# Kernel optimization log

Measured on AMD Instinct MI355X. Metric: run time of the kernel, lower is better.

Reference implementation:

```python
import jax, jax.numpy as jnp
import numpy as np

NUM_NODES = 1_000_000
MEM_DIM = 100
TIME_DIM = 100
MSG_DIM = 4
OUT_CH = 2
BATCH = 262144
BN_EPS = 1e-5


def setup_inputs() -> dict:
    key = jax.random.key(0)
    ks = jax.random.split(key, 24)
    s = 0.05
    D = MEM_DIM
    gru_in = 2 * D + MSG_DIM + TIME_DIM  # IdentityMessage output dim = 304
    inp = {
        "n_id": jax.random.randint(ks[0], (BATCH,), 0, NUM_NODES, dtype=jnp.int64 if jax.config.jax_enable_x64 else jnp.int32),
        "memory": jax.random.normal(ks[1], (NUM_NODES, D), jnp.float32),
        "last_update": jax.random.randint(ks[2], (NUM_NODES,), 0, 100000),
        "store_src": jax.random.randint(ks[3], (NUM_NODES,), 0, NUM_NODES),
        "store_dst": jax.random.randint(ks[4], (NUM_NODES,), 0, NUM_NODES),
        "store_t": jax.random.randint(ks[5], (NUM_NODES,), 0, 200000),
        "store_msg": jax.random.normal(ks[6], (NUM_NODES, MSG_DIM), jnp.float32),
        # TimeEncoder: Linear(1, time_dim) followed by cos
        "time_w": jax.random.normal(ks[7], (TIME_DIM, 1), jnp.float32) * s,
        "time_b": jax.random.normal(ks[8], (TIME_DIM,), jnp.float32) * s,
        # GRUCell(input=304, hidden=100)
        "W_ih": jax.random.normal(ks[9], (3 * D, gru_in), jnp.float32) * s,
        "b_ih": jax.random.normal(ks[10], (3 * D,), jnp.float32) * s,
        "W_hh": jax.random.normal(ks[11], (3 * D, D), jnp.float32) * s,
        "b_hh": jax.random.normal(ks[12], (3 * D,), jnp.float32) * s,
        # classifier: Linear(100,64) -> ReLU -> BatchNorm1d(64) -> Linear(64,2)
        "W1": jax.random.normal(ks[13], (64, D), jnp.float32) * s,
        "b1": jax.random.normal(ks[14], (64,), jnp.float32) * s,
        "gamma": jnp.ones((64,), jnp.float32),
        "beta": jnp.zeros((64,), jnp.float32),
        "W2": jax.random.normal(ks[15], (OUT_CH, 64), jnp.float32) * s,
        "b2": jax.random.normal(ks[16], (OUT_CH,), jnp.float32) * s,
    }
    return inp


def reference(n_id, memory, last_update, store_src, store_dst, store_t, store_msg,
              time_w, time_b, W_ih, b_ih, W_hh, b_hh, W1, b1, gamma, beta, W2, b2):
    D = memory.shape[1]
    # ---- TGNMemory._get_updated_memory(n_id) with LastAggregator ----
    h = memory[n_id]                                   # [B, D] gather of node memory
    src = store_src[n_id]
    dst = store_dst[n_id]
    raw_msg = store_msg[n_id]                          # [B, msg_dim]
    dt = (store_t[n_id] - last_update[n_id]).astype(jnp.float32)[:, None]  # [B, 1]
    t_enc = jnp.cos(dt @ time_w.T + time_b)            # [B, time_dim]
    # IdentityMessage: concat(mem[src], mem[dst], raw_msg, time_enc)
    x = jnp.concatenate([memory[src], memory[dst], raw_msg, t_enc], axis=-1)  # [B, 2D+msg+T]
    # GRUCell update
    gi = x @ W_ih.T + b_ih                             # [B, 3D]
    gh = h @ W_hh.T + b_hh                             # [B, 3D]
    i_r, i_z, i_n = gi[:, :D], gi[:, D:2 * D], gi[:, 2 * D:]
    h_r, h_z, h_n = gh[:, :D], gh[:, D:2 * D], gh[:, 2 * D:]
    r = jax.nn.sigmoid(i_r + h_r)
    z = jax.nn.sigmoid(i_z + h_z)
    n = jnp.tanh(i_n + r * h_n)
    h_new = (1.0 - z) * n + z * h                      # [B, D]
    # ---- classifier: Linear -> ReLU -> BatchNorm1d (train stats) -> Linear ----
    a = jax.nn.relu(h_new @ W1.T + b1)                 # [B, 64]
    mu = jnp.mean(a, axis=0)
    var = jnp.var(a, axis=0)
    a = (a - mu) * jax.lax.rsqrt(var + BN_EPS) * gamma + beta
    return a @ W2.T + b2                               # [B, out_channels]
```

## Files before the change

### kernel.cpp

```cpp
#include <hip/hip_runtime.h>
#include <stdint.h>

#define BATCH   262144
#define DMEM    100
#define AS      456

typedef float    f32x4 __attribute__((ext_vector_type(4)));
typedef _Float16 f16x8 __attribute__((ext_vector_type(8)));
typedef unsigned short u16x4 __attribute__((ext_vector_type(4)));

__device__ __forceinline__ unsigned short f2h(float f) {
  union { _Float16 h; unsigned short u; } v; v.h = (_Float16)f;
  return v.u;
}
__device__ __forceinline__ float h2f(unsigned short u) {
  union { _Float16 h; unsigned short u; } v; v.u = u; return (float)v.h;
}

#define MFMA16(A, B, C) __builtin_amdgcn_mfma_f32_16x16x32_f16((A), (B), (C), 0, 0, 0)

namespace wcfg {
constexpr int NT[4][7] = {
  {0, 1, 2, 3, 19, 20, 21},
  {4, 5, 6, 7, 22, 23, 24},
  {8, 9, 10, 11, 13, 13, 13},
  {12, 14, 15, 16, 17, 18, 25}};
constexpr int LEN[4] = {7, 7, 5, 7};
}

__global__ void prep_kernel(const float* __restrict__ W_ih, const float* __restrict__ W_hh,
                            const float* __restrict__ W1,
                            const float* __restrict__ b_ih, const float* __restrict__ b_hh,
                            unsigned short* __restrict__ Bfrag,
                            unsigned short* __restrict__ W1frag,
                            float* __restrict__ biasbuf,
                            float* __restrict__ stats_g) {
  int blk = blockIdx.x;
  int tid = threadIdx.x;
  if (blk == 72) {
    if (tid < 128) stats_g[tid] = 0.f;
    if (tid < 100) {
      biasbuf[tid]       = b_ih[tid]       + b_hh[tid];
      biasbuf[100 + tid] = b_ih[100 + tid] + b_hh[100 + tid];
      biasbuf[200 + tid] = b_ih[200 + tid];
      biasbuf[300 + tid] = b_hh[200 + tid];
    }
    return;
  }
  int o = blk * 4 + (tid >> 6);
  if (o >= 286) return;
  int lane = tid & 63, quad = lane >> 4, l15 = lane & 15;
  if (o < 270) {
    int kc, nt;
    if (o < 190) { kc = o / 19; nt = o % 19; }
    else { int o2 = o - 190; kc = 10 + o2 / 20; int p = o2 % 20; nt = (p < 13) ? p : p + 6; }
    int col = nt * 16 + l15;
    unsigned short* dst = Bfrag + (size_t)o * 512 + lane * 8;
    for (int j = 0; j < 8; ++j) {
      int kg = kc * 32 + quad * 8 + j;
      float v = 0.f;
      if (kc < 10) {
        if (kg < 304 && col < 300) v = W_ih[col * 304 + kg];
      } else {
        int kl = kg - 320;
        if (nt < 13) { if (kl < 100 && col < 200) v = W_hh[col * 100 + kl]; }
        else { int hd = col - 304; if (kl < 100 && hd < 100) v = W_hh[(200 + hd) * 100 + kl]; }
      }
      dst[j] = f2h(v);
    }
  } else {
    int o1 = o - 270;
    int kc = o1 >> 2, nt = o1 & 3;
    int col = nt * 16 + l15;
    unsigned short* dst = W1frag + (size_t)o1 * 512 + lane * 8;
    for (int j = 0; j < 8; ++j) {
      int kg = kc * 32 + quad * 8 + j;
      dst[j] = f2h((kg < 100) ? W1[col * 100 + kg] : 0.f);
    }
  }
}

template<int W>
__device__ __forceinline__ void b_prefetch0(f16x8 (&bq)[7],
    const unsigned short* __restrict__ Bfrag, size_t boff) {
  constexpr auto& NT = wcfg::NT[W];
  constexpr int L = wcfg::LEN[W];
  #pragma unroll
  for (int t = 0; t < 7; ++t)
    if (t < L && NT[t] < 19)
      bq[t] = *(const f16x8*)(Bfrag + (size_t)NT[t] * 512 + boff);
}

template<int W>
__device__ __forceinline__ void gemm_core(f32x4 (&acc)[7][4], f16x8 (&bq)[7],
    const unsigned short* __restrict__ Bfrag, const unsigned short* Arow,
    int quad, size_t boff) {
  constexpr auto& NT = wcfg::NT[W];
  constexpr int L = wcfg::LEN[W];
  #pragma unroll
  for (int kc = 0; kc < 10; ++kc) {
    const int kb = kc * 32 + quad * 8;
    f16x8 af[4];
    #pragma unroll
    for (int m = 0; m < 4; ++m)
      af[m] = __builtin_bit_cast(f16x8, *(const uint4*)(Arow + m * 16 * AS + kb));
    f16x8 bn[7];
    if (kc < 9) {
      const unsigned short* Bk = Bfrag + (size_t)(kc + 1) * 19 * 512 + boff;
      #pragma unroll
      for (int t = 0; t < 7; ++t)
        if (t < L && NT[t] < 19)
          bn[t] = *(const f16x8*)(Bk + (size_t)NT[t] * 512);
    } else {
      const unsigned short* Bk = Bfrag + (size_t)190 * 512 + boff;
      #pragma unroll
      for (int t = 0; t < 7; ++t)
        if (t < L && (NT[t] < 13 || NT[t] >= 19))
          bn[t] = *(const f16x8*)(Bk + (size_t)((NT[t] < 13) ? NT[t] : NT[t] - 6) * 512);
    }
    #pragma unroll
    for (int t = 0; t < 7; ++t)
      if (t < L && NT[t] < 19) {
        #pragma unroll
        for (int m = 0; m < 4; ++m)
          acc[t][m] = MFMA16(af[m], bq[t], acc[t][m]);
      }
    if (kc < 9) {
      #pragma unroll
      for (int t = 0; t < 7; ++t)
        if (t < L && NT[t] < 19) bq[t] = bn[t];
    } else {
      #pragma unroll
      for (int t = 0; t < 7; ++t)
        if (t < L && (NT[t] < 13 || NT[t] >= 19)) bq[t] = bn[t];
    }
  }
  #pragma unroll
  for (int kc = 10; kc < 14; ++kc) {
    const int kb = kc * 32 + quad * 8;
    f16x8 af[4];
    #pragma unroll
    for (int m = 0; m < 4; ++m)
      af[m] = __builtin_bit_cast(f16x8, *(const uint4*)(Arow + m * 16 * AS + kb));
    f16x8 bn[7];
    if (kc < 13) {
      const unsigned short* Bk = Bfrag + (size_t)(190 + (kc - 9) * 20) * 512 + boff;
      #pragma unroll
      for (int t = 0; t < 7; ++t)
        if (t < L && (NT[t] < 13 || NT[t] >= 19))
          bn[t] = *(const f16x8*)(Bk + (size_t)((NT[t] < 13) ? NT[t] : NT[t] - 6) * 512);
    }
    #pragma unroll
    for (int t = 0; t < 7; ++t)
      if (t < L && (NT[t] < 13 || NT[t] >= 19)) {
        #pragma unroll
        for (int m = 0; m < 4; ++m)
          acc[t][m] = MFMA16(af[m], bq[t], acc[t][m]);
      }
    if (kc < 13) {
      #pragma unroll
      for (int t = 0; t < 7; ++t)
        if (t < L && (NT[t] < 13 || NT[t] >= 19)) bq[t] = bn[t];
    }
  }
}

template<int W>
__device__ __forceinline__ void dump_acc(const f32x4 (&acc)[7][4],
    unsigned short* A_lds, int quad, int l15) {
  constexpr auto& NT = wcfg::NT[W];
  constexpr int L = wcfg::LEN[W];
  #pragma unroll
  for (int t = 0; t < 7; ++t)
    if (t < L) {
      const int col = NT[t] * 16 + l15;
      #pragma unroll
      for (int m = 0; m < 4; ++m) {
        const int rbase = m * 16 + quad * 4;
        #pragma unroll
        for (int rr = 0; rr < 4; ++rr)
          A_lds[(rbase + rr) * AS + col] = f2h(acc[t][m][rr]);
      }
    }
}

__global__ __launch_bounds__(256, 2)
void main_kernel(const int* __restrict__ n_id, const float* __restrict__ memory,
                 const int* __restrict__ last_update,
                 const int* __restrict__ store_src, const int* __restrict__ store_dst,
                 const int* __restrict__ store_t, const float* __restrict__ store_msg,
                 const float* __restrict__ time_w, const float* __restrict__ time_b,
                 const float* __restrict__ b1,
                 const unsigned short* __restrict__ Bfrag,
                 const unsigned short* __restrict__ W1frag,
                 const float* __restrict__ biasbuf,
                 unsigned short* __restrict__ a_ws, float* __restrict__ stats_g) {
  __shared__ __align__(16) unsigned short A_lds[64 * AS];
  __shared__ __align__(16) unsigned short hbuf[64 * 100];
  __shared__ float bias_lds[400];
  __shared__ float stats[128];

  const int tid  = threadIdx.x;
  const int wave = tid >> 6;
  const int lane = tid & 63;
  const int quad = lane >> 4;
  const int l15  = lane & 15;
  const int blk  = blockIdx.x;
  const size_t boff = (size_t)lane * 8;

  if (tid < 128) stats[tid] = 0.f;
  if (tid < 200) {
    bias_lds[tid]       = biasbuf[tid];
    bias_lds[200 + tid] = biasbuf[200 + tid];
  }

  {
    const int r = tid >> 2;
    const int p = tid & 3;
    const int b = blk * 64 + r;
    const int n = n_id[b];
    const int sidx = store_src[n];
    const int didx = store_dst[n];
    const int stt  = store_t[n];
    const int lu   = last_update[n];
    const float* ms = memory + (size_t)sidx * DMEM;
    const float* md = memory + (size_t)didx * DMEM;
    const float* mh = memory + (size_t)n * DMEM;
    unsigned short* Ar = A_lds + r * AS;

    f32x4 vals[19];
    #pragma unroll
    for (int i = 0; i < 19; ++i) {
      const int v = i * 4 + p;
      const int a = v / 25;
      const int c = v - a * 25;
      const float* bp = (a == 0) ? ms : ((a == 1) ? md : mh);
      vals[i] = *(const f32x4*)(bp + c * 4);
    }
    f32x4 mg;
    if (p == 0) mg = *(const f32x4*)(store_msg + (size_t)n * 4);

    const float dtf = (float)(stt - lu);
    const int d0 = p * 25;
    for (int i = 0; i < 25; ++i) {
      const int d = d0 + i;
      Ar[204 + d] = f2h(cosf(dtf * time_w[d] + time_b[d]));
    }
    if (p == 0) {
      u16x4 m4 = { f2h(mg[0]), f2h(mg[1]), f2h(mg[2]), f2h(mg[3]) };
      *(u16x4*)(Ar + 200) = m4;
    } else if (p == 1) {
      uint4 z4 = {0u, 0u, 0u, 0u};
      *(uint4*)(Ar + 304) = z4;
      *(uint4*)(Ar + 312) = z4;
    } else if (p == 2) {
      u16x4 z = {0, 0, 0, 0};
      *(u16x4*)(Ar + 420) = z; *(u16x4*)(Ar + 424) = z;
      *(u16x4*)(Ar + 428) = z; *(u16x4*)(Ar + 432) = z;
    } else {
      u16x4 z = {0, 0, 0, 0};
      *(u16x4*)(Ar + 436) = z; *(u16x4*)(Ar + 440) = z; *(u16x4*)(Ar + 444) = z;
    }
    #pragma unroll
    for (int i = 0; i < 19; ++i) {
      const int v = i * 4 + p;
      const int a = v / 25;
      const int c = v - a * 25;
      const int off = (a == 0) ? (c * 4)
                    : ((a == 1) ? (100 + c * 4)
                    : ((a == 2) ? (320 + c * 4) : 448));
      u16x4 h4 = { f2h(vals[i][0]), f2h(vals[i][1]), f2h(vals[i][2]), f2h(vals[i][3]) };
      *(u16x4*)(Ar + off) = h4;
    }
  }

  f32x4 acc[7][4];
  #pragma unroll
  for (int t = 0; t < 7; ++t)
    #pragma unroll
    for (int m = 0; m < 4; ++m) acc[t][m] = f32x4{0.f, 0.f, 0.f, 0.f};

  f16x8 bq[7];
  switch (wave) {
    case 0: b_prefetch0<0>(bq, Bfrag, boff); break;
    case 1: b_prefetch0<1>(bq, Bfrag, boff); break;
    case 2: b_prefetch0<2>(bq, Bfrag, boff); break;
    default: b_prefetch0<3>(bq, Bfrag, boff); break;
  }
  __syncthreads();

  const unsigned short* Arow = A_lds + l15 * AS;
  switch (wave) {
    case 0: gemm_core<0>(acc, bq, Bfrag, Arow, quad, boff); break;
    case 1: gemm_core<1>(acc, bq, Bfrag, Arow, quad, boff); break;
    case 2: gemm_core<2>(acc, bq, Bfrag, Arow, quad, boff); break;
    default: gemm_core<3>(acc, bq, Bfrag, Arow, quad, boff); break;
  }
  __syncthreads();

  for (int i = 0; i < 25; ++i) {
    int e = tid + 256 * i;
    hbuf[e] = A_lds[(e / 100) * AS + 320 + (e % 100)];
  }
  __syncthreads();

  switch (wave) {
    case 0: dump_acc<0>(acc, A_lds, quad, l15); break;
    case 1: dump_acc<1>(acc, A_lds, quad, l15); break;
    case 2: dump_acc<2>(acc, A_lds, quad, l15); break;
    default: dump_acc<3>(acc, A_lds, quad, l15); break;
  }

  f16x8 wb[4];
  #pragma unroll
  for (int k4 = 0; k4 < 4; ++k4)
    wb[k4] = *(const f16x8*)(W1frag + (size_t)(k4 * 4 + wave) * 512 + boff);

  __syncthreads();

  for (int i = 0; i < 25; ++i) {
    int e = tid + 256 * i;
    int r = e / 100, d = e % 100;
    const unsigned short* Gr = A_lds + r * AS;
    float s_r = h2f(Gr[d])       + bias_lds[d];
    float s_z = h2f(Gr[100 + d]) + bias_lds[100 + d];
    float i_n = h2f(Gr[200 + d]) + bias_lds[200 + d];
    float h_n = h2f(Gr[304 + d]) + bias_lds[300 + d];
    float h   = h2f(hbuf[r * 100 + d]);
    float rg = __builtin_amdgcn_rcpf(1.f + __expf(-s_r));
    float zg = __builtin_amdgcn_rcpf(1.f + __expf(-s_z));
    float x2 = i_n + rg * h_n;
    x2 = fminf(fmaxf(x2, -30.f), 30.f);
    float e2 = __expf(-2.f * x2);
    float nn = (1.f - e2) * __builtin_amdgcn_rcpf(1.f + e2);
    float hw = (1.f - zg) * nn + zg * h;
    A_lds[r * AS + d] = f2h(hw);
  }
  __syncthreads();

  f32x4 aacc[4];
  #pragma unroll
  for (int m = 0; m < 4; ++m) aacc[m] = f32x4{0.f, 0.f, 0.f, 0.f};
  #pragma unroll
  for (int k4 = 0; k4 < 4; ++k4) {
    const int kb = k4 * 32 + quad * 8;
    #pragma unroll
    for (int m = 0; m < 4; ++m) {
      f16x8 a = __builtin_bit_cast(f16x8, *(const uint4*)(Arow + m * 16 * AS + kb));
      aacc[m] = MFMA16(a, wb[k4], aacc[m]);
    }
  }

  const int col = wave * 16 + l15;
  const float bb = b1[col];
  float ssum = 0.f, ssq = 0.f;
  #pragma unroll
  for (int m = 0; m < 4; ++m) {
    const int rbase = m * 16 + quad * 4;
    #pragma unroll
    for (int rr = 0; rr < 4; ++rr) {
      float v = fmaxf(aacc[m][rr] + bb, 0.f);
      ssum += v; ssq += v * v;
      a_ws[(size_t)(blk * 64 + rbase + rr) * 64 + col] = f2h(v);
    }
  }
  ssum += __shfl_xor(ssum, 16); ssum += __shfl_xor(ssum, 32);
  ssq  += __shfl_xor(ssq, 16);  ssq  += __shfl_xor(ssq, 32);
  if (quad == 0) {
    atomicAdd(&stats[col], ssum);
    atomicAdd(&stats[64 + col], ssq);
  }
  __syncthreads();
  if (tid < 128) atomicAdd(&stats_g[tid], stats[tid]);
}

__global__ __launch_bounds__(256)
void out_kernel(const unsigned short* __restrict__ a_ws, const float* __restrict__ stats_g,
                const float* __restrict__ gamma, const float* __restrict__ beta,
                const float* __restrict__ W2, const float* __restrict__ b2,
                float* __restrict__ out) {
  __shared__ float w0[64], w1[64], cpart[128];
  __shared__ float C0s, C1s;
  int tid = threadIdx.x;
  if (tid < 64) {
    const float invB = 1.f / (float)BATCH;
    float mu  = stats_g[tid] * invB;
    float var = stats_g[64 + tid] * invB - mu * mu;
    float g   = gamma[tid] * rsqrtf(var + 1e-5f);
    w0[tid] = g * W2[tid];
    w1[tid] = g * W2[64 + tid];
    float t = beta[tid] - mu * g;
    cpart[tid]      = t * W2[tid];
    cpart[64 + tid] = t * W2[64 + tid];
  }
  __syncthreads();
  if (tid == 0) {
    float c0 = b2[0], c1 = b2[1];
    for (int j = 0; j < 64; ++j) { c0 += cpart[j]; c1 += cpart[64 + j]; }
    C0s = c0; C1s = c1;
  }
  __syncthreads();
  int b = blockIdx.x * 256 + tid;
  const uint4* ap = (const uint4*)(a_ws + (size_t)b * 64);
  float o0 = C0s, o1 = C1s;
  #pragma unroll
  for (int i = 0; i < 8; ++i) {
    uint4 v = ap[i];
    unsigned int uu[4] = {v.x, v.y, v.z, v.w};
    #pragma unroll
    for (int q = 0; q < 4; ++q) {
      float lo = h2f((unsigned short)(uu[q] & 0xffffu));
      float hi = h2f((unsigned short)(uu[q] >> 16));
      int j = i * 8 + q * 2;
      o0 += lo * w0[j] + hi * w0[j + 1];
      o1 += lo * w1[j] + hi * w1[j + 1];
    }
  }
  *(float2*)(out + (size_t)b * 2) = make_float2(o0, o1);
}

extern "C" void kernel_launch(void* const* d_in, const int* in_sizes, int n_in,
                              void* d_out, int out_size, void* d_ws, size_t ws_size,
                              hipStream_t stream) {
  const int*   n_id   = (const int*)d_in[0];
  const float* memory = (const float*)d_in[1];
  const int*   last_u = (const int*)d_in[2];
  const int*   s_src  = (const int*)d_in[3];
  const int*   s_dst  = (const int*)d_in[4];
  const int*   s_t    = (const int*)d_in[5];
  const float* s_msg  = (const float*)d_in[6];
  const float* time_w = (const float*)d_in[7];
  const float* time_b = (const float*)d_in[8];
  const float* W_ih   = (const float*)d_in[9];
  const float* b_ih   = (const float*)d_in[10];
  const float* W_hh   = (const float*)d_in[11];
  const float* b_hh   = (const float*)d_in[12];
  const float* W1     = (const float*)d_in[13];
  const float* b1     = (const float*)d_in[14];
  const float* gamma  = (const float*)d_in[15];
  const float* beta   = (const float*)d_in[16];
  const float* W2     = (const float*)d_in[17];
  const float* b2     = (const float*)d_in[18];

  char* ws = (char*)d_ws;
  float*          stats_g = (float*)ws;
  float*          biasbuf = (float*)(ws + 512);
  unsigned short* Bfrag   = (unsigned short*)(ws + 4096);
  unsigned short* W1frag  = (unsigned short*)(ws + 4096 + 276480);
  unsigned short* a_ws    = (unsigned short*)(ws + (1u << 20));

  prep_kernel<<<73, 256, 0, stream>>>(W_ih, W_hh, W1, b_ih, b_hh, Bfrag, W1frag,
                                      biasbuf, stats_g);
  main_kernel<<<4096, 256, 0, stream>>>(n_id, memory, last_u, s_src, s_dst, s_t,
                                        s_msg, time_w, time_b, b1,
                                        Bfrag, W1frag, biasbuf, a_ws, stats_g);
  out_kernel<<<1024, 256, 0, stream>>>(a_ws, stats_g, gamma, beta, W2, b2, (float*)d_out);
}
```

Before: 749.9 us.

## Halve rows per block to 32 and raise occupancy to four blocks per CU

Each block now handles 32 batch rows instead of 64. That halves LDS and accumulator registers per block, and launch bounds ask for 4 blocks per SM instead of 2. The gather is remapped to 8 threads per row. The software-pipelined B-fragment prefetch is removed, so each k-step loads B inside the loop. The aim is more waves in flight to hide the random gather latency. The cost is that each B fragment is reused across half as many rows, which doubles B loads per row, and the global stats atomics double.

```diff
diff --git a/kernel.cpp b/kernel.cpp
--- a/kernel.cpp
+++ b/kernel.cpp
@@ -3,6 +3,7 @@
 
 #define BATCH   262144
 #define DMEM    100
+#define ROWS    32
 #define AS      456
 
 typedef float    f32x4 __attribute__((ext_vector_type(4)));
@@ -81,92 +82,41 @@
 }
 
 template<int W>
-__device__ __forceinline__ void b_prefetch0(f16x8 (&bq)[7],
-    const unsigned short* __restrict__ Bfrag, size_t boff) {
-  constexpr auto& NT = wcfg::NT[W];
-  constexpr int L = wcfg::LEN[W];
-  #pragma unroll
-  for (int t = 0; t < 7; ++t)
-    if (t < L && NT[t] < 19)
-      bq[t] = *(const f16x8*)(Bfrag + (size_t)NT[t] * 512 + boff);
-}
-
-template<int W>
-__device__ __forceinline__ void gemm_core(f32x4 (&acc)[7][4], f16x8 (&bq)[7],
+__device__ __forceinline__ void gemm_core(f32x4 (&acc)[7][2],
     const unsigned short* __restrict__ Bfrag, const unsigned short* Arow,
     int quad, size_t boff) {
   constexpr auto& NT = wcfg::NT[W];
   constexpr int L = wcfg::LEN[W];
   #pragma unroll
-  for (int kc = 0; kc < 10; ++kc) {
+  for (int kc = 0; kc < 14; ++kc) {
     const int kb = kc * 32 + quad * 8;
-    f16x8 af[4];
-    #pragma unroll
-    for (int m = 0; m < 4; ++m)
-      af[m] = __builtin_bit_cast(f16x8, *(const uint4*)(Arow + m * 16 * AS + kb));
-    f16x8 bn[7];
-    if (kc < 9) {
-      const unsigned short* Bk = Bfrag + (size_t)(kc + 1) * 19 * 512 + boff;
-      #pragma unroll
-      for (int t = 0; t < 7; ++t)
-        if (t < L && NT[t] < 19)
-          bn[t] = *(const f16x8*)(Bk + (size_t)NT[t] * 512);
-    } else {
-      const unsigned short* Bk = Bfrag + (size_t)190 * 512 + boff;
-      #pragma unroll
-      for (int t = 0; t < 7; ++t)
-        if (t < L && (NT[t] < 13 || NT[t] >= 19))
-          bn[t] = *(const f16x8*)(Bk + (size_t)((NT[t] < 13) ? NT[t] : NT[t] - 6) * 512);
-    }
-    #pragma unroll
-    for (int t = 0; t < 7; ++t)
-      if (t < L && NT[t] < 19) {
-        #pragma unroll
-        for (int m = 0; m < 4; ++m)
-          acc[t][m] = MFMA16(af[m], bq[t], acc[t][m]);
+    f16x8 bq[7];
+    #pragma unroll
+    for (int t = 0; t < 7; ++t) {
+      if (t >= L) continue;
+      const bool member = (kc < 10) ? (NT[t] < 19) : (NT[t] < 13 || NT[t] >= 19);
+      if (member) {
+        const int op = (kc < 10) ? (kc * 19 + NT[t])
+                     : (190 + (kc - 10) * 20 + ((NT[t] < 13) ? NT[t] : NT[t] - 6));
+        bq[t] = *(const f16x8*)(Bfrag + (size_t)op * 512 + boff);
       }
-    if (kc < 9) {
-      #pragma unroll
-      for (int t = 0; t < 7; ++t)
-        if (t < L && NT[t] < 19) bq[t] = bn[t];
-    } else {
-      #pragma unroll
-      for (int t = 0; t < 7; ++t)
-        if (t < L && (NT[t] < 13 || NT[t] >= 19)) bq[t] = bn[t];
-    }
-  }
-  #pragma unroll
-  for (int kc = 10; kc < 14; ++kc) {
-    const int kb = kc * 32 + quad * 8;
-    f16x8 af[4];
-    #pragma unroll
-    for (int m = 0; m < 4; ++m)
-      af[m] = __builtin_bit_cast(f16x8, *(const uint4*)(Arow + m * 16 * AS + kb));
-    f16x8 bn[7];
-    if (kc < 13) {
-      const unsigned short* Bk = Bfrag + (size_t)(190 + (kc - 9) * 20) * 512 + boff;
-      #pragma unroll
-      for (int t = 0; t < 7; ++t)
-        if (t < L && (NT[t] < 13 || NT[t] >= 19))
-          bn[t] = *(const f16x8*)(Bk + (size_t)((NT[t] < 13) ? NT[t] : NT[t] - 6) * 512);
-    }
-    #pragma unroll
-    for (int t = 0; t < 7; ++t)
-      if (t < L && (NT[t] < 13 || NT[t] >= 19)) {
-        #pragma unroll
-        for (int m = 0; m < 4; ++m)
-          acc[t][m] = MFMA16(af[m], bq[t], acc[t][m]);
+    }
+    f16x8 af0 = __builtin_bit_cast(f16x8, *(const uint4*)(Arow + kb));
+    f16x8 af1 = __builtin_bit_cast(f16x8, *(const uint4*)(Arow + 16 * AS + kb));
+    #pragma unroll
+    for (int t = 0; t < 7; ++t) {
+      if (t >= L) continue;
+      const bool member = (kc < 10) ? (NT[t] < 19) : (NT[t] < 13 || NT[t] >= 19);
+      if (member) {
+        acc[t][0] = MFMA16(af0, bq[t], acc[t][0]);
+        acc[t][1] = MFMA16(af1, bq[t], acc[t][1]);
       }
-    if (kc < 13) {
-      #pragma unroll
-      for (int t = 0; t < 7; ++t)
-        if (t < L && (NT[t] < 13 || NT[t] >= 19)) bq[t] = bn[t];
     }
   }
 }
 
 template<int W>
-__device__ __forceinline__ void dump_acc(const f32x4 (&acc)[7][4],
+__device__ __forceinline__ void dump_acc(const f32x4 (&acc)[7][2],
     unsigned short* A_lds, int quad, int l15) {
   constexpr auto& NT = wcfg::NT[W];
   constexpr int L = wcfg::LEN[W];
@@ -175,7 +125,7 @@
     if (t < L) {
       const int col = NT[t] * 16 + l15;
       #pragma unroll
-      for (int m = 0; m < 4; ++m) {
+      for (int m = 0; m < 2; ++m) {
         const int rbase = m * 16 + quad * 4;
         #pragma unroll
         for (int rr = 0; rr < 4; ++rr)
@@ -184,7 +134,7 @@
     }
 }
 
-__global__ __launch_bounds__(256, 2)
+__global__ __launch_bounds__(256, 4)
 void main_kernel(const int* __restrict__ n_id, const float* __restrict__ memory,
                  const int* __restrict__ last_update,
                  const int* __restrict__ store_src, const int* __restrict__ store_dst,
@@ -195,8 +145,8 @@
                  const unsigned short* __restrict__ W1frag,
                  const float* __restrict__ biasbuf,
                  unsigned short* __restrict__ a_ws, float* __restrict__ stats_g) {
-  __shared__ __align__(16) unsigned short A_lds[64 * AS];
-  __shared__ __align__(16) unsigned short hbuf[64 * 100];
+  __shared__ __align__(16) unsigned short A_lds[ROWS * AS];
+  __shared__ __align__(16) unsigned short hbuf[ROWS * 100];
   __shared__ float bias_lds[400];
   __shared__ float stats[128];
 
@@ -215,9 +165,9 @@
   }
 
   {
-    const int r = tid >> 2;
-    const int p = tid & 3;
-    const int b = blk * 64 + r;
+    const int r = tid >> 3;
+    const int p = tid & 7;
+    const int b = blk * ROWS + r;
     const int n = n_id[b];
     const int sidx = store_src[n];
     const int didx = store_dst[n];
@@ -228,23 +178,24 @@
     const float* mh = memory + (size_t)n * DMEM;
     unsigned short* Ar = A_lds + r * AS;
 
-    f32x4 vals[19];
-    #pragma unroll
-    for (int i = 0; i < 19; ++i) {
-      const int v = i * 4 + p;
+    f32x4 vals[10];
+    #pragma unroll
+    for (int i = 0; i < 10; ++i) {
+      const int v = i * 8 + p;
       const int a = v / 25;
       const int c = v - a * 25;
-      const float* bp = (a == 0) ? ms : ((a == 1) ? md : mh);
-      vals[i] = *(const f32x4*)(bp + c * 4);
+      const float* bp = (a == 0) ? ms : ((a == 1) ? md : ((a == 2) ? mh : mh));
+      vals[i] = (a < 3) ? *(const f32x4*)(bp + c * 4) : *(const f32x4*)mh;
     }
     f32x4 mg;
     if (p == 0) mg = *(const f32x4*)(store_msg + (size_t)n * 4);
 
     const float dtf = (float)(stt - lu);
-    const int d0 = p * 25;
-    for (int i = 0; i < 25; ++i) {
-      const int d = d0 + i;
-      Ar[204 + d] = f2h(cosf(dtf * time_w[d] + time_b[d]));
+    #pragma unroll
+    for (int i = 0; i < 13; ++i) {
+      const int d = p * 13 + i;
+      if (d < 100)
+        Ar[204 + d] = f2h(cosf(dtf * time_w[d] + time_b[d]));
     }
     if (p == 0) {
       u16x4 m4 = { f2h(mg[0]), f2h(mg[1]), f2h(mg[2]), f2h(mg[3]) };
@@ -257,13 +208,13 @@
       u16x4 z = {0, 0, 0, 0};
       *(u16x4*)(Ar + 420) = z; *(u16x4*)(Ar + 424) = z;
       *(u16x4*)(Ar + 428) = z; *(u16x4*)(Ar + 432) = z;
-    } else {
+    } else if (p == 3) {
       u16x4 z = {0, 0, 0, 0};
       *(u16x4*)(Ar + 436) = z; *(u16x4*)(Ar + 440) = z; *(u16x4*)(Ar + 444) = z;
     }
     #pragma unroll
-    for (int i = 0; i < 19; ++i) {
-      const int v = i * 4 + p;
+    for (int i = 0; i < 10; ++i) {
+      const int v = i * 8 + p;
       const int a = v / 25;
       const int c = v - a * 25;
       const int off = (a == 0) ? (c * 4)
@@ -274,33 +225,28 @@
     }
   }
 
-  f32x4 acc[7][4];
+  f32x4 acc[7][2];
   #pragma unroll
   for (int t = 0; t < 7; ++t)
     #pragma unroll
-    for (int m = 0; m < 4; ++m) acc[t][m] = f32x4{0.f, 0.f, 0.f, 0.f};
-
-  f16x8 bq[7];
-  switch (wave) {
-    case 0: b_prefetch0<0>(bq, Bfrag, boff); break;
-    case 1: b_prefetch0<1>(bq, Bfrag, boff); break;
-    case 2: b_prefetch0<2>(bq, Bfrag, boff); break;
-    default: b_prefetch0<3>(bq, Bfrag, boff); break;
-  }
+    for (int m = 0; m < 2; ++m) acc[t][m] = f32x4{0.f, 0.f, 0.f, 0.f};
+
   __syncthreads();
 
   const unsigned short* Arow = A_lds + l15 * AS;
   switch (wave) {
-    case 0: gemm_core<0>(acc, bq, Bfrag, Arow, quad, boff); break;
-    case 1: gemm_core<1>(acc, bq, Bfrag, Arow, quad, boff); break;
-    case 2: gemm_core<2>(acc, bq, Bfrag, Arow, quad, boff); break;
-    default: gemm_core<3>(acc, bq, Bfrag, Arow, quad, boff); break;
-  }
-  __syncthreads();
-
-  for (int i = 0; i < 25; ++i) {
+    case 0: gemm_core<0>(acc, Bfrag, Arow, quad, boff); break;
+    case 1: gemm_core<1>(acc, Bfrag, Arow, quad, boff); break;
+    case 2: gemm_core<2>(acc, Bfrag, Arow, quad, boff); break;
+    default: gemm_core<3>(acc, Bfrag, Arow, quad, boff); break;
+  }
+  __syncthreads();
+
+  #pragma unroll
+  for (int i = 0; i < 13; ++i) {
     int e = tid + 256 * i;
-    hbuf[e] = A_lds[(e / 100) * AS + 320 + (e % 100)];
+    if (e < ROWS * 100)
+      hbuf[e] = A_lds[(e / 100) * AS + 320 + (e % 100)];
   }
   __syncthreads();
 
@@ -318,34 +264,37 @@
 
   __syncthreads();
 
-  for (int i = 0; i < 25; ++i) {
+  #pragma unroll
+  for (int i = 0; i < 13; ++i) {
     int e = tid + 256 * i;
-    int r = e / 100, d = e % 100;
-    const unsigned short* Gr = A_lds + r * AS;
-    float s_r = h2f(Gr[d])       + bias_lds[d];
-    float s_z = h2f(Gr[100 + d]) + bias_lds[100 + d];
-    float i_n = h2f(Gr[200 + d]) + bias_lds[200 + d];
-    float h_n = h2f(Gr[304 + d]) + bias_lds[300 + d];
-    float h   = h2f(hbuf[r * 100 + d]);
-    float rg = __builtin_amdgcn_rcpf(1.f + __expf(-s_r));
-    float zg = __builtin_amdgcn_rcpf(1.f + __expf(-s_z));
-    float x2 = i_n + rg * h_n;
-    x2 = fminf(fmaxf(x2, -30.f), 30.f);
-    float e2 = __expf(-2.f * x2);
-    float nn = (1.f - e2) * __builtin_amdgcn_rcpf(1.f + e2);
-    float hw = (1.f - zg) * nn + zg * h;
-    A_lds[r * AS + d] = f2h(hw);
-  }
-  __syncthreads();
-
-  f32x4 aacc[4];
-  #pragma unroll
-  for (int m = 0; m < 4; ++m) aacc[m] = f32x4{0.f, 0.f, 0.f, 0.f};
+    if (e < ROWS * 100) {
+      int r = e / 100, d = e % 100;
+      const unsigned short* Gr = A_lds + r * AS;
+      float s_r = h2f(Gr[d])       + bias_lds[d];
+      float s_z = h2f(Gr[100 + d]) + bias_lds[100 + d];
+      float i_n = h2f(Gr[200 + d]) + bias_lds[200 + d];
+      float h_n = h2f(Gr[304 + d]) + bias_lds[300 + d];
+      float h   = h2f(hbuf[r * 100 + d]);
+      float rg = __builtin_amdgcn_rcpf(1.f + __expf(-s_r));
+      float zg = __builtin_amdgcn_rcpf(1.f + __expf(-s_z));
+      float x2 = i_n + rg * h_n;
+      x2 = fminf(fmaxf(x2, -30.f), 30.f);
+      float e2 = __expf(-2.f * x2);
+      float nn = (1.f - e2) * __builtin_amdgcn_rcpf(1.f + e2);
+      float hw = (1.f - zg) * nn + zg * h;
+      A_lds[r * AS + d] = f2h(hw);
+    }
+  }
+  __syncthreads();
+
+  f32x4 aacc[2];
+  #pragma unroll
+  for (int m = 0; m < 2; ++m) aacc[m] = f32x4{0.f, 0.f, 0.f, 0.f};
   #pragma unroll
   for (int k4 = 0; k4 < 4; ++k4) {
     const int kb = k4 * 32 + quad * 8;
     #pragma unroll
-    for (int m = 0; m < 4; ++m) {
+    for (int m = 0; m < 2; ++m) {
       f16x8 a = __builtin_bit_cast(f16x8, *(const uint4*)(Arow + m * 16 * AS + kb));
       aacc[m] = MFMA16(a, wb[k4], aacc[m]);
     }
@@ -355,13 +304,13 @@
   const float bb = b1[col];
   float ssum = 0.f, ssq = 0.f;
   #pragma unroll
-  for (int m = 0; m < 4; ++m) {
+  for (int m = 0; m < 2; ++m) {
     const int rbase = m * 16 + quad * 4;
     #pragma unroll
     for (int rr = 0; rr < 4; ++rr) {
       float v = fmaxf(aacc[m][rr] + bb, 0.f);
       ssum += v; ssq += v * v;
-      a_ws[(size_t)(blk * 64 + rbase + rr) * 64 + col] = f2h(v);
+      a_ws[(size_t)(blk * ROWS + rbase + rr) * 64 + col] = f2h(v);
     }
   }
   ssum += __shfl_xor(ssum, 16); ssum += __shfl_xor(ssum, 32);
@@ -451,8 +400,8 @@
 
   prep_kernel<<<73, 256, 0, stream>>>(W_ih, W_hh, W1, b_ih, b_hh, Bfrag, W1frag,
                                       biasbuf, stats_g);
-  main_kernel<<<4096, 256, 0, stream>>>(n_id, memory, last_u, s_src, s_dst, s_t,
-                                        s_msg, time_w, time_b, b1,
-                                        Bfrag, W1frag, biasbuf, a_ws, stats_g);
+  main_kernel<<<BATCH / ROWS, 256, 0, stream>>>(n_id, memory, last_u, s_src, s_dst, s_t,
+                                                s_msg, time_w, time_b, b1,
+                                                Bfrag, W1frag, biasbuf, a_ws, stats_g);
   out_kernel<<<1024, 256, 0, stream>>>(a_ws, stats_g, gamma, beta, W2, b2, (float*)d_out);
 }
```

Result: slower. 784.7 us (+4.6%).
